# Kernel tuning notes

Measured on AMD Instinct MI355X. Metric: run time of the kernel, lower is better.

## Reference

```python
import math
import jax, jax.numpy as jnp
import numpy as np

FNUM = 64      # exp_channels (fnum)
NHEADS = 4     # num_heads
WS = 8         # window size (both spatial dims)
SHIFT = 4      # cyclic shift (hard-coded in module)
SCALE = FNUM ** -0.5   # NOTE: module scales by fnum**-0.5, not head_dim**-0.5
LN_EPS = 1e-5


def sine_pos_encoding(h, w, num_pos_feats, temperature=10000.0):
    # DETR-style normalized sine position encoding -> (1, h*w, 2*num_pos_feats)
    scale = 2.0 * math.pi
    y = np.cumsum(np.ones((1, h, w), dtype=np.float64), axis=1)
    x = np.cumsum(np.ones((1, h, w), dtype=np.float64), axis=2)
    eps = 1e-6
    y = y / (y[:, -1:, :] + eps) * scale
    x = x / (x[:, :, -1:] + eps) * scale
    dim_t = np.arange(num_pos_feats, dtype=np.float64)
    dim_t = temperature ** (2.0 * (dim_t // 2) / num_pos_feats)
    pos_x = x[..., None] / dim_t
    pos_y = y[..., None] / dim_t
    pos_x = np.stack([np.sin(pos_x[..., 0::2]), np.cos(pos_x[..., 1::2])], axis=-1).reshape(1, h, w, -1)
    pos_y = np.stack([np.sin(pos_y[..., 0::2]), np.cos(pos_y[..., 1::2])], axis=-1).reshape(1, h, w, -1)
    pos = np.concatenate([pos_y, pos_x], axis=-1)
    return jnp.asarray(pos.reshape(1, h * w, 2 * num_pos_feats), dtype=jnp.float32)


def compute_mask_np(H, W, ws, ss):
    # Swin shifted-window attention mask -> (nW, ws*ws, ws*ws) with 0 / -100
    img = np.zeros((H, W))
    cnt = 0
    for hs in (slice(0, -ws), slice(-ws, -ss), slice(-ss, None)):
        for wsl in (slice(0, -ws), slice(-ws, -ss), slice(-ss, None)):
            img[hs, wsl] = cnt
            cnt += 1
    mw = img.reshape(H // ws, ws, W // ws, ws).transpose(0, 2, 1, 3).reshape(-1, ws * ws)
    diff = mw[:, None, :] - mw[:, :, None]
    return jnp.asarray(np.where(diff != 0, -100.0, 0.0), dtype=jnp.float32)


def layernorm(x, w, b):
    m = x.mean(-1, keepdims=True)
    v = x.var(-1, keepdims=True)
    return (x - m) * jax.lax.rsqrt(v + LN_EPS) * w + b


def window_attention(q, k, v, mask):
    # q,k,v: (Bw, nH, N, Ch); mask: (nW, N, N)
    att = jnp.einsum('bhnc,bhmc->bhnm', q * SCALE, k)
    nW, N = mask.shape[0], mask.shape[1]
    att = att.reshape(-1, nW, NHEADS, N, N) + mask[None, :, None]
    att = jax.nn.softmax(att.reshape(-1, NHEADS, N, N), axis=-1)
    out = jnp.einsum('bhnm,bhmc->bnhc', att, v)   # merge heads as (nH C)
    return out.reshape(out.shape[0], N, -1)


def merge_heads(q):
    # (Bw, nH, N, Ch) -> (Bw, N, nH*Ch)
    return q.transpose(0, 2, 1, 3).reshape(q.shape[0], q.shape[2], -1)


def geglu(h, w11, b11, w12, b12, w2, b2):
    return (jax.nn.gelu(h @ w11 + b11, approximate=False) * (h @ w12 + b12)) @ w2 + b2


def reference(x, ln1_w, ln1_b, ln2_w, ln2_b, w_qkv, me_w11, me_b11, me_w12, me_b12, me_w2, me_b2, conv11_w, ff_in_w, ff_dw_w, ff_out_w):
    B, _, C, H, W = x.shape
    nHw, nWw = H // WS, W // WS
    nW = nHw * nWw
    N = WS * WS
    Ch = FNUM // NHEADS
    pos = sine_pos_encoding(WS, WS, FNUM // 2)
    mask = compute_mask_np(H, W, WS, SHIFT)
    x0 = x
    xs = jnp.roll(x, (-SHIFT, -SHIFT), axis=(3, 4))
    # window partition: (B,3,C,H,W) -> (B*3*nW, N, C)
    xw = xs.reshape(B, 3, C, nHw, WS, nWw, WS).transpose(0, 1, 3, 5, 4, 6, 2).reshape(-1, N, C)
    xw = layernorm(xw, ln1_w, ln1_b)
    qkv = (xw + pos) @ w_qkv                                   # (B*3*nW, N, 3F)
    # '(B E nW) W (nP C) -> E nP (B nW) W C'
    qkv = qkv.reshape(B, 3, nW, N, 3, FNUM).transpose(1, 4, 0, 2, 3, 5).reshape(3, 3, B * nW, N, FNUM)
    # '(C nH)' head split: head index is the fast axis (faithful to source)
    qkv = qkv.reshape(3, 3, B * nW, N, Ch, NHEADS).transpose(0, 1, 2, 5, 3, 4)  # (E, P, Bw, nH, N, Ch)
    a1 = window_attention(qkv[1, 0], qkv[0, 1], qkv[0, 2], mask)
    a3 = window_attention(qkv[1, 0], qkv[2, 1], qkv[2, 2], mask)
    a21 = window_attention(qkv[0, 0], qkv[1, 1], qkv[1, 2], mask)
    a21b = window_attention(qkv[0, 0], qkv[2, 1], qkv[2, 2], mask)
    a23 = window_attention(qkv[2, 0], qkv[1, 1], qkv[1, 2], mask)
    a23b = window_attention(qkv[2, 0], qkv[0, 1], qkv[0, 2], mask)
    # keep_query=True path: concat attended features with own query, GEGLU per exposure
    h1 = geglu(jnp.concatenate([a21, a21b, merge_heads(qkv[0, 0])], -1), me_w11[0], me_b11[0], me_w12[0], me_b12[0], me_w2[0], me_b2[0])
    h2 = geglu(jnp.concatenate([a1, a3, merge_heads(qkv[1, 0])], -1), me_w11[1], me_b11[1], me_w12[1], me_b12[1], me_w2[1], me_b2[1])
    h3 = geglu(jnp.concatenate([a23, a23b, merge_heads(qkv[2, 0])], -1), me_w11[2], me_b11[2], me_w12[2], me_b12[2], me_w2[2], me_b2[2])
    xc = jnp.concatenate([h1, h2, h3], 0)                      # (3*B*nW, N, F)
    # window reverse + ffn_dconv 1x1 conv across 3F channels
    xr = xc.reshape(3, B, nHw, nWw, WS, WS, FNUM).transpose(1, 0, 6, 2, 4, 3, 5).reshape(B, 3 * FNUM, H, W)
    xr = jnp.einsum('oi,bihw->bohw', conv11_w, xr).reshape(B, 3, FNUM, H, W)
    xr = jnp.roll(xr, (SHIFT, SHIFT), axis=(3, 4))
    xres = xr + x0
    # FFN: LN over (N C), then GEGLU dwconv FeedForward
    xl = layernorm(xres.transpose(0, 3, 4, 1, 2).reshape(B, H, W, 3 * FNUM), ln2_w, ln2_b)
    xcn = xl.transpose(0, 3, 1, 2)                             # (B, 3F, H, W)
    h = jnp.einsum('oi,bihw->bohw', ff_in_w, xcn)              # (B, 12F, H, W)
    h = jax.lax.conv_general_dilated(h, ff_dw_w[:, None], (1, 1), ((1, 1), (1, 1)),
                                     feature_group_count=h.shape[1],
                                     dimension_numbers=('NCHW', 'OIHW', 'NCHW'))
    g1, g2 = jnp.split(h, 2, axis=1)
    h = jax.nn.gelu(g1, approximate=False) * g2                # (B, 6F, H, W)
    out = jnp.einsum('oi,bihw->bohw', ff_out_w, h).reshape(B, 3, FNUM, H, W)
    return xres + out


def setup_inputs():
    key = jax.random.key(0)
    ks = jax.random.split(key, 10)
    F3, F6, F12 = 3 * FNUM, 6 * FNUM, 12 * FNUM
    def w(k, shape, fan_in):
        return jax.random.normal(k, shape, jnp.float32) * (fan_in ** -0.5)
    return {
        'x': jax.random.normal(ks[0], (1, 3, FNUM, 256, 256), jnp.float32),
        'ln1_w': jnp.ones((FNUM,), jnp.float32),
        'ln1_b': jnp.zeros((FNUM,), jnp.float32),
        'ln2_w': jnp.ones((F3,), jnp.float32),
        'ln2_b': jnp.zeros((F3,), jnp.float32),
        'w_qkv': w(ks[1], (FNUM, F3), FNUM),
        'me_w11': w(ks[2], (3, F3, FNUM), F3),
        'me_b11': jnp.zeros((3, FNUM), jnp.float32),
        'me_w12': w(ks[3], (3, F3, FNUM), F3),
        'me_b12': jnp.zeros((3, FNUM), jnp.float32),
        'me_w2': w(ks[4], (3, FNUM, FNUM), FNUM),
        'me_b2': jnp.zeros((3, FNUM), jnp.float32),
        'conv11_w': w(ks[5], (F3, F3), F3),
        'ff_in_w': w(ks[6], (F12, F3), F3),
        'ff_dw_w': w(ks[7], (F12, 3, 3), 9),
        'ff_out_w': w(ks[8], (F3, F6), F6),
    }
```

## Files before the change

kernel.cpp:

```cpp
#include <hip/hip_runtime.h>
#include <hip/hip_bf16.h>
#include <math.h>

typedef __hip_bfloat16 bf16;
typedef __attribute__((ext_vector_type(8))) short short8;
typedef __attribute__((ext_vector_type(4))) short short4v;
typedef __attribute__((ext_vector_type(4))) float f32x4;

__device__ __forceinline__ float b2f(bf16 v) { return __bfloat162float(v); }
__device__ __forceinline__ bf16 f2b(float v) { return __float2bfloat16(v); }
__device__ __forceinline__ short f2s(float v) { bf16 b = __float2bfloat16(v); return *(short*)&b; }
__device__ __forceinline__ float s2f(short s) { bf16 b = *(bf16*)&s; return __bfloat162float(b); }
__device__ __forceinline__ float gelu_fast(float x) {
  float z = 0.7978845608028654f * x * (1.0f + 0.044715f * x * x);
  float e = __expf(2.0f * z);
  float t = 1.0f - 2.0f / (e + 1.0f);
  return 0.5f * x * (1.0f + t);
}
__device__ __forceinline__ bool detect_f32(const void* ln1w) {
  return *(const unsigned int*)ln1w == 0x3F800000u;
}
__device__ __forceinline__ float ldx(const void* p, int i, bool f32) {
  return f32 ? ((const float*)p)[i] : b2f(((const bf16*)p)[i]);
}
#define MFMA16(a, b, c) __builtin_amdgcn_mfma_f32_16x16x32_bf16((a), (b), (c), 0, 0, 0)

#define OFF_LN1W  0
#define OFF_LN1B  64
#define OFF_LN2W  128
#define OFF_LN2B  320
#define OFF_WQKVT 512
#define OFF_W11T  12800
#define OFF_B11   49664
#define OFF_W12T  49856
#define OFF_B12   86720
#define OFF_W2T   86912
#define OFF_B2    99200
#define OFF_CW    99392
#define OFF_FIW   136256
#define OFF_DWW   283712
#define OFF_FOW   290624

#define QOFF 0
#define KOFF 4352
#define VOFF 9472

__global__ void __launch_bounds__(256) k_convert(
    const void* __restrict__ src, bf16* __restrict__ dst, int n,
    const void* __restrict__ raw) {
  const bool f32 = detect_f32(raw);
  int i = blockIdx.x * 256 + threadIdx.x;
  if (i < n) dst[i] = f2b(ldx(src, i, f32));
}

__global__ void __launch_bounds__(256) k_convT(
    const void* __restrict__ src, bf16* __restrict__ dst, int R, int C, int n,
    const void* __restrict__ raw) {
  const bool f32 = detect_f32(raw);
  int i = blockIdx.x * 256 + threadIdx.x;
  if (i >= n) return;
  int rc = R * C;
  int s = i / rc, rem = i - s * rc;
  int r = rem / C, c = rem - r * C;
  dst[s * rc + c * R + r] = f2b(ldx(src, i, f32));
}

__global__ void __launch_bounds__(256) k_pos(float* __restrict__ posT) {
  int i = blockIdx.x * 256 + threadIdx.x;
  if (i >= 4096) return;
  int t = i >> 6, ch = i & 63;
  int r = t >> 3, c = t & 7;
  int c2 = ch & 31;
  float coord = (ch < 32) ? (float)(r + 1) : (float)(c + 1);
  float base = coord * (6.283185307179586f / 8.000001f);
  int k = c2 >> 1;
  float d = powf(10000.0f, (float)k * (1.0f / 16.0f));
  float a = base / d;
  posT[i] = (c2 & 1) ? cosf(a) : sinf(a);
}

__global__ void __launch_bounds__(256) k_qkv(
    const void* __restrict__ x, const void* __restrict__ raw,
    const bf16* __restrict__ W, const float* __restrict__ posT,
    short* __restrict__ qkvS, int wy0, int NWL) {
  const int e  = blockIdx.x / NWL;
  const int wl = blockIdx.x - e * NWL;
  const int wy = wy0 + (wl >> 5), wx = wl & 31;
  const int tid = threadIdx.x;
  const bool xf32 = detect_f32(raw);

  __shared__ alignas(16) short xln[64 * 72];
  __shared__ alignas(16) short qout[13824];
  __shared__ float mu[64], rs[64];

  for (int i = tid; i < 1024; i += 256) {
    int xq = i & 1, ty = (i >> 1) & 7, ch = i >> 4;
    int y  = (wy * 8 + ty + 4) & 255;
    int xs = (wx * 8 + 4 + xq * 4) & 255;
    size_t gi = ((size_t)(e * 64 + ch) * 256 + y) * 256 + xs;
    float f0, f1, f2, f3;
    if (xf32) {
      f32x4 v4 = *(const f32x4*)((const float*)x + gi);
      f0 = v4[0]; f1 = v4[1]; f2 = v4[2]; f3 = v4[3];
    } else {
      short4v v4 = *(const short4v*)((const bf16*)x + gi);
      f0 = s2f(v4[0]); f1 = s2f(v4[1]); f2 = s2f(v4[2]); f3 = s2f(v4[3]);
    }
    int tb = (ty * 8 + xq * 4) * 72 + ch;
    xln[tb]       = f2s(f0);
    xln[tb + 72]  = f2s(f1);
    xln[tb + 144] = f2s(f2);
    xln[tb + 216] = f2s(f3);
  }
  __syncthreads();
  if (tid < 64) {
    const short* row = xln + tid * 72;
    float s = 0.f, s2 = 0.f;
    #pragma unroll
    for (int k8 = 0; k8 < 8; k8++) {
      short8 v = *(const short8*)(row + k8 * 8);
      #pragma unroll
      for (int j = 0; j < 8; j++) { float f = s2f(v[j]); s += f; s2 += f * f; }
    }
    float m = s * (1.0f / 64.0f);
    float var = s2 * (1.0f / 64.0f) - m * m;
    mu[tid] = m; rs[tid] = rsqrtf(var + 1e-5f);
  }
  __syncthreads();
  for (int u = tid; u < 512; u += 256) {
    int co = u & 7, t = u >> 3;
    int idx = t * 72 + co * 8;
    short8 xv = *(const short8*)(xln + idx);
    float m = mu[t], rr = rs[t];
    const float* pt = posT + t * 64 + co * 8;
    f32x4 pa = *(const f32x4*)pt;
    f32x4 pb = *(const f32x4*)(pt + 4);
    short8 lw = *(const short8*)(const void*)(W + OFF_LN1W + co * 8);
    short8 lb = *(const short8*)(const void*)(W + OFF_LN1B + co * 8);
    short8 o;
    #pragma unroll
    for (int j = 0; j < 8; j++) {
      float p = (j < 4) ? pa[j] : pb[j - 4];
      o[j] = f2s((s2f(xv[j]) - m) * rr * s2f(lw[j]) + s2f(lb[j]) + p);
    }
    *(short8*)(xln + idx) = o;
  }
  __syncthreads();

  const int lid = tid & 63;
  const int w = tid >> 6;
  const int mrow = lid & 15, q = lid >> 4;
  const int t0 = w * 16 + q * 4;
  const int h = mrow & 3;
  const bf16* wqT = W + OFF_WQKVT;
  short8 a0 = *(const short8*)(xln + (w * 16 + mrow) * 72 + q * 8);
  short8 a1 = *(const short8*)(xln + (w * 16 + mrow) * 72 + 32 + q * 8);
  for (int nt = 0; nt < 12; nt++) {
    f32x4 acc = {0.f, 0.f, 0.f, 0.f};
    short8 b0 = *(const short8*)(const void*)(wqT + (nt * 16 + mrow) * 64 + q * 8);
    short8 b1 = *(const short8*)(const void*)(wqT + (nt * 16 + mrow) * 64 + 32 + q * 8);
    acc = MFMA16(a0, b0, acc);
    acc = MFMA16(a1, b1, acc);
    int p = nt >> 2;
    int c = (nt & 3) * 4 + (mrow >> 2);
    if (p == 0) {
      int o2 = h * 16 + c;
      #pragma unroll
      for (int r = 0; r < 4; r++)
        qout[QOFF + (t0 + r) * 68 + o2] = f2s(acc[r]);
    } else if (p == 1) {
      int rb = KOFF + (h * 64 + t0) * 20 + c;
      #pragma unroll
      for (int r = 0; r < 4; r++)
        qout[rb + r * 20] = f2s(acc[r] * 0.125f);
    } else {
      int rb = VOFF + (h * 16 + c) * 68 + q * 16 + w;
      #pragma unroll
      for (int r = 0; r < 4; r++)
        qout[rb + r * 4] = f2s(acc[r]);
    }
  }
  __syncthreads();
  const size_t gb = ((size_t)wl * 9 + e * 3) * 4096;
  for (int u = tid; u < 3072; u += 256) {
    int j = u * 4, p = j >> 12, rem = j & 4095, src;
    if (p == 0)      src = QOFF + (rem >> 6) * 68 + (rem & 63);
    else if (p == 1) src = KOFF + (rem >> 4) * 20 + (rem & 15);
    else             src = VOFF + (rem >> 6) * 68 + (rem & 63);
    *(short4v*)(qkvS + gb + j) = *(const short4v*)(qout + src);
  }
}

__global__ void __launch_bounds__(256, 3) k_attn(
    const short* __restrict__ qkvS, const bf16* __restrict__ W,
    short* __restrict__ xcS, int wy0, int NWL) {
  const int e  = blockIdx.x / NWL;
  const int wl = blockIdx.x - e * NWL;
  const int wy = wy0 + (wl >> 5), wx = wl & 31;
  const int tid = threadIdx.x;

  __shared__ alignas(16) short cat[64 * 200];
  __shared__ alignas(16) short Kh[4096];
  __shared__ alignas(16) short Vt[64 * 72];
  __shared__ alignas(16) short Pb[64 * 72];
  __shared__ alignas(16) short kz[16];
  short* gbuf = Pb;

  const int ea = (e == 0) ? 1 : ((e == 1) ? 0 : 1);
  const int eb = (e == 0) ? 2 : ((e == 1) ? 2 : 0);
  const short* Qg = qkvS + ((size_t)wl * 9 + e * 3 + 0) * 4096;
  const short* Kg[2] = { qkvS + ((size_t)wl * 9 + ea * 3 + 1) * 4096,
                         qkvS + ((size_t)wl * 9 + eb * 3 + 1) * 4096 };
  const short* Vg[2] = { qkvS + ((size_t)wl * 9 + ea * 3 + 2) * 4096,
                         qkvS + ((size_t)wl * 9 + eb * 3 + 2) * 4096 };

  if (tid < 16) kz[tid] = 0;
  for (int i = tid; i < 512; i += 256) {
    int t = i >> 3, ch = i & 7;
    *(short8*)(cat + t * 200 + 128 + ch * 8) = *(const short8*)(Qg + t * 64 + ch * 8);
  }

  const int lid = tid & 63;
  const int w = tid >> 6;
  const int mrow = lid & 15, q = lid >> 4;
  const int masky = (wy == 31), maskx = (wx == 31);
  const bool anymask = (masky | maskx) != 0;
  const short8 zero8 = {0, 0, 0, 0, 0, 0, 0, 0};

  float madd[4][4];
  if (anymask) {
    int qi = w * 16 + mrow;
    int lyi = masky ? (((qi >> 3) < 4) ? 1 : 2) : 0;
    int lxi = maskx ? (((qi & 7) < 4) ? 1 : 2) : 0;
    #pragma unroll
    for (int nt = 0; nt < 4; nt++)
      #pragma unroll
      for (int r = 0; r < 4; r++) {
        int kj = nt * 16 + q * 4 + r;
        int lyj = masky ? (((kj >> 3) < 4) ? 1 : 2) : 0;
        int lxj = maskx ? (((kj & 7) < 4) ? 1 : 2) : 0;
        madd[nt][r] = (lyi != lyj || lxi != lxj) ? -100.0f : 0.0f;
      }
  }

  for (int src = 0; src < 2; src++) {
    if (src) __syncthreads();
    for (int i = tid; i < 512; i += 256)
      *(short8*)(Kh + i * 8) = *(const short8*)(Kg[src] + i * 8);
    for (int i = tid; i < 512; i += 256) {
      int row = i >> 3, ch = i & 7;
      *(short8*)(Vt + row * 72 + ch * 8) = *(const short8*)(Vg[src] + row * 64 + ch * 8);
    }
    __syncthreads();

    for (int h = 0; h < 4; h++) {
      short8 qf = (q < 2)
          ? *(const short8*)(cat + (w * 16 + mrow) * 200 + 128 + h * 16 + q * 8)
          : zero8;
      const short* kb; int kstep;
      if (q < 2) { kb = Kh + (h * 64 + mrow) * 16 + q * 8; kstep = 256; }
      else       { kb = kz; kstep = 0; }
      f32x4 s[4];
      #pragma unroll
      for (int nt = 0; nt < 4; nt++) {
        short8 kf = *(const short8*)(kb + nt * kstep);
        f32x4 z = {0.f, 0.f, 0.f, 0.f};
        s[nt] = MFMA16(kf, qf, z);
      }
      if (anymask) {
        #pragma unroll
        for (int nt = 0; nt < 4; nt++)
          #pragma unroll
          for (int r = 0; r < 4; r++) s[nt][r] += madd[nt][r];
      }
      float mx = s[0][0];
      #pragma unroll
      for (int nt = 0; nt < 4; nt++)
        #pragma unroll
        for (int r = 0; r < 4; r++) if (nt | r) mx = fmaxf(mx, s[nt][r]);
      mx = fmaxf(mx, __shfl_xor(mx, 16));
      mx = fmaxf(mx, __shfl_xor(mx, 32));
      float pr[4][4]; float sum = 0.f;
      #pragma unroll
      for (int nt = 0; nt < 4; nt++)
        #pragma unroll
        for (int r = 0; r < 4; r++) {
          float ev = __expf(s[nt][r] - mx);
          pr[nt][r] = ev; sum += ev;
        }
      sum += __shfl_xor(sum, 16);
      sum += __shfl_xor(sum, 32);
      float inv = 1.0f / sum;
      int ro = (w * 16 + mrow) * 72 + q * 16;
      #pragma unroll
      for (int r = 0; r < 4; r++) {
        short4v pv = { f2s(pr[0][r] * inv), f2s(pr[1][r] * inv),
                       f2s(pr[2][r] * inv), f2s(pr[3][r] * inv) };
        *(short4v*)(Pb + ro + r * 4) = pv;
      }
      asm volatile("s_waitcnt lgkmcnt(0)" ::: "memory");
      f32x4 o = {0.f, 0.f, 0.f, 0.f};
      #pragma unroll
      for (int kc = 0; kc < 2; kc++) {
        short8 pa = *(const short8*)(Pb + (w * 16 + mrow) * 72 + kc * 32 + q * 8);
        short8 vb = *(const short8*)(Vt + (h * 16 + mrow) * 72 + kc * 32 + q * 8);
        o = MFMA16(pa, vb, o);
      }
      #pragma unroll
      for (int r = 0; r < 4; r++)
        cat[(w * 16 + q * 4 + r) * 200 + src * 64 + h * 16 + mrow] = f2s(o[r]);
    }
  }
  __syncthreads();

  {
    short8 a[6];
    #pragma unroll
    for (int kc = 0; kc < 6; kc++)
      a[kc] = *(const short8*)(cat + (w * 16 + mrow) * 200 + kc * 32 + q * 8);
    f32x4 ua[4], va[4];
    const bf16* w1T = W + OFF_W11T + (size_t)e * 64 * 192;
    const bf16* w2T = W + OFF_W12T + (size_t)e * 64 * 192;
    for (int nt = 0; nt < 4; nt++) {
      f32x4 au = {0.f, 0.f, 0.f, 0.f}, av = {0.f, 0.f, 0.f, 0.f};
      #pragma unroll
      for (int kc = 0; kc < 6; kc++) {
        short8 bu = *(const short8*)(const void*)(w1T + (nt * 16 + mrow) * 192 + kc * 32 + q * 8);
        short8 bv = *(const short8*)(const void*)(w2T + (nt * 16 + mrow) * 192 + kc * 32 + q * 8);
        au = MFMA16(a[kc], bu, au);
        av = MFMA16(a[kc], bv, av);
      }
      ua[nt] = au; va[nt] = av;
    }
    for (int nt = 0; nt < 4; nt++) {
      int o = nt * 16 + mrow;
      float bu = b2f(W[OFF_B11 + e * 64 + o]);
      float bv = b2f(W[OFF_B12 + e * 64 + o]);
      #pragma unroll
      for (int r = 0; r < 4; r++)
        gbuf[(w * 16 + q * 4 + r) * 72 + o] = f2s(gelu_fast(ua[nt][r] + bu) * (va[nt][r] + bv));
    }
  }
  {
    short8 g0 = *(const short8*)(gbuf + (w * 16 + mrow) * 72 + q * 8);
    short8 g1 = *(const short8*)(gbuf + (w * 16 + mrow) * 72 + 32 + q * 8);
    const bf16* w2T = W + OFF_W2T + (size_t)e * 64 * 64;
    for (int nt = 0; nt < 4; nt++) {
      f32x4 acc = {0.f, 0.f, 0.f, 0.f};
      short8 b0 = *(const short8*)(const void*)(w2T + (nt * 16 + mrow) * 64 + q * 8);
      short8 b1 = *(const short8*)(const void*)(w2T + (nt * 16 + mrow) * 64 + 32 + q * 8);
      acc = MFMA16(g0, b0, acc);
      acc = MFMA16(g1, b1, acc);
      int o = nt * 16 + mrow;
      float bb = b2f(W[OFF_B2 + e * 64 + o]);
      #pragma unroll
      for (int r = 0; r < 4; r++)
        cat[(w * 16 + q * 4 + r) * 200 + o] = f2s(acc[r] + bb);
    }
  }
  __syncthreads();
  short* xcbase = xcS + ((size_t)wl * 3 + e) * 4096;
  for (int i = tid; i < 1024; i += 256) {
    int tt = i >> 4, f4 = (i & 15) * 4;
    *(short4v*)(xcbase + tt * 64 + f4) = *(const short4v*)(cat + tt * 200 + f4);
  }
}

__global__ void __launch_bounds__(256) k_conv11(
    const short* __restrict__ xcS, const bf16* __restrict__ W,
    const void* __restrict__ x, const void* __restrict__ raw,
    short* __restrict__ xres, int wy0, int NWL) {
  const int wl = blockIdx.x;
  const int wy = wy0 + (wl >> 5), wx = wl & 31;
  const int tid = threadIdx.x;
  const bool xf32 = detect_f32(raw);
  __shared__ alignas(16) short ct[64 * 200];
  __shared__ alignas(16) short xt[64 * 200];

  for (int i = tid; i < 3072; i += 256) {
    int e = i >> 10, rem = i & 1023;
    int tt = rem >> 4, f4 = (rem & 15) * 4;
    *(short4v*)(ct + tt * 200 + e * 64 + f4)
        = *(const short4v*)(xcS + ((size_t)wl * 3 + e) * 4096 + tt * 64 + f4);
  }
  for (int i = tid; i < 3072; i += 256) {
    int xq = i & 1, ty = (i >> 1) & 7, ch = (i >> 4) & 63, e = i >> 10;
    int y  = (wy * 8 + ty + 4) & 255;
    int xs = (wx * 8 + 4 + xq * 4) & 255;
    size_t gi = ((size_t)(e * 64 + ch) * 256 + y) * 256 + xs;
    float f0, f1, f2, f3;
    if (xf32) {
      f32x4 v4 = *(const f32x4*)((const float*)x + gi);
      f0 = v4[0]; f1 = v4[1]; f2 = v4[2]; f3 = v4[3];
    } else {
      short4v v4 = *(const short4v*)((const bf16*)x + gi);
      f0 = s2f(v4[0]); f1 = s2f(v4[1]); f2 = s2f(v4[2]); f3 = s2f(v4[3]);
    }
    int tb = (ty * 8 + xq * 4) * 200 + e * 64 + ch;
    xt[tb]       = f2s(f0);
    xt[tb + 200] = f2s(f1);
    xt[tb + 400] = f2s(f2);
    xt[tb + 600] = f2s(f3);
  }
  __syncthreads();

  const int lid = tid & 63;
  const int w = tid >> 6;
  const int mrow = lid & 15, q = lid >> 4;
  short8 a[6];
  #pragma unroll
  for (int kc = 0; kc < 6; kc++)
    a[kc] = *(const short8*)(ct + (w * 16 + mrow) * 200 + kc * 32 + q * 8);

  const int t = w * 16 + mrow;
  const int ty2 = (wy * 8 + (t >> 3) + 4) & 255;
  const int tx2 = (wx * 8 + (t & 7) + 4) & 255;
  short* xrow = xres + (size_t)(ty2 * 256 + tx2) * 192;
  const short* resrow = xt + t * 200;

  const bf16* cw = W + OFF_CW;
  for (int nt = 0; nt < 12; nt++) {
    f32x4 acc = {0.f, 0.f, 0.f, 0.f};
    #pragma unroll
    for (int kc = 0; kc < 6; kc++) {
      short8 b = *(const short8*)(const void*)(cw + (nt * 16 + mrow) * 192 + kc * 32 + q * 8);
      acc = MFMA16(b, a[kc], acc);
    }
    int o = nt * 16 + q * 4;
    short4v rv = *(const short4v*)(resrow + o);
    short4v o4 = { f2s(acc[0] + s2f(rv[0])), f2s(acc[1] + s2f(rv[1])),
                   f2s(acc[2] + s2f(rv[2])), f2s(acc[3] + s2f(rv[3])) };
    *(short4v*)(xrow + o) = o4;
  }
}

__global__ void __launch_bounds__(256) k_ffin(
    const short* __restrict__ xres, const bf16* __restrict__ W,
    short* __restrict__ hS, int y_start, int y0m1) {
  const int half = blockIdx.x & 1;
  const int idx = blockIdx.x >> 1;
  const int y = y_start + (idx >> 2);
  const int x0 = (idx & 3) * 64;
  const int l = y - y0m1;
  const int tid = threadIdx.x;
  __shared__ alignas(16) short xt[64 * 200];
  __shared__ float mu[64], rs[64];

  for (int i4 = tid; i4 < 3072; i4 += 256) {
    int p = i4 / 48, c4 = (i4 - p * 48) * 4;
    *(short4v*)(xt + p * 200 + c4)
        = *(const short4v*)(xres + (size_t)(y * 256 + x0 + p) * 192 + c4);
  }
  __syncthreads();
  {
    int p = tid >> 2, qd = tid & 3;
    const short* row = xt + p * 200 + qd * 48;
    float s = 0.f, s2 = 0.f;
    #pragma unroll
    for (int k = 0; k < 6; k++) {
      short8 v = *(const short8*)(row + k * 8);
      #pragma unroll
      for (int j = 0; j < 8; j++) { float f = s2f(v[j]); s += f; s2 += f * f; }
    }
    s  += __shfl_xor(s, 1);  s  += __shfl_xor(s, 2);
    s2 += __shfl_xor(s2, 1); s2 += __shfl_xor(s2, 2);
    if (qd == 0) {
      float m = s * (1.0f / 192.0f);
      float var = s2 * (1.0f / 192.0f) - m * m;
      mu[p] = m; rs[p] = rsqrtf(var + 1e-5f);
    }
  }
  __syncthreads();
  for (int u = tid; u < 1536; u += 256) {
    int p = u / 24, c8 = u - p * 24;
    int idx2 = p * 200 + c8 * 8;
    short8 xv = *(const short8*)(xt + idx2);
    float m = mu[p], rr = rs[p];
    short8 lw = *(const short8*)(const void*)(W + OFF_LN2W + c8 * 8);
    short8 lb = *(const short8*)(const void*)(W + OFF_LN2B + c8 * 8);
    short8 o;
    #pragma unroll
    for (int j = 0; j < 8; j++)
      o[j] = f2s((s2f(xv[j]) - m) * rr * s2f(lw[j]) + s2f(lb[j]));
    *(short8*)(xt + idx2) = o;
  }
  __syncthreads();

  const int lid = tid & 63;
  const int m0 = (tid >> 6) * 16;
  const int mrow = lid & 15, q = lid >> 4;
  short8 a[6];
  #pragma unroll
  for (int kc = 0; kc < 6; kc++)
    a[kc] = *(const short8*)(xt + (m0 + mrow) * 200 + kc * 32 + q * 8);

  const bf16* fiw = W + OFF_FIW;
  short* hrow = hS + (size_t)l * 196608 + (size_t)(x0 + m0 + mrow) * 768;
  const int nt0 = half * 24;
  for (int nt = nt0; nt < nt0 + 24; nt++) {
    f32x4 acc = {0.f, 0.f, 0.f, 0.f};
    #pragma unroll
    for (int kc = 0; kc < 6; kc++) {
      short8 b = *(const short8*)(const void*)(fiw + (nt * 16 + mrow) * 192 + kc * 32 + q * 8);
      acc = MFMA16(b, a[kc], acc);
    }
    short4v o4 = { f2s(acc[0]), f2s(acc[1]), f2s(acc[2]), f2s(acc[3]) };
    *(short4v*)(hrow + nt * 16 + q * 4) = o4;
  }
}

__global__ void __launch_bounds__(256) k_ffout(
    const short* __restrict__ hS, const bf16* __restrict__ W,
    const short* __restrict__ xres, void* __restrict__ out,
    const void* __restrict__ raw, int y0, int y0m1) {
  const int y = y0 + (blockIdx.x >> 2);
  const int x0 = (blockIdx.x & 3) * 64;
  const int tid = threadIdx.x;
  const bool of32 = detect_f32(raw);
  __shared__ alignas(16) short ga[64 * 392];

  const bf16* dwwT = W + OFF_DWW;
  const int l = y - y0m1;
  const short8 z8 = {0, 0, 0, 0, 0, 0, 0, 0};
  for (int it = 0; it < 6; it++) {
    int unit = it * 256 + tid;
    int pq = unit / 48, oo = unit - pq * 48;
    int o = oo * 8;
    int xxb = x0 + pq * 2;
    float u0[8] = {0,0,0,0,0,0,0,0}, v0[8] = {0,0,0,0,0,0,0,0};
    float u1[8] = {0,0,0,0,0,0,0,0}, v1[8] = {0,0,0,0,0,0,0,0};
    #pragma unroll
    for (int dy = -1; dy <= 1; dy++) {
      int yy = y + dy;
      if (yy < 0 || yy >= 256) continue;
      const short* rbase = hS + (size_t)(l + dy) * 196608;
      short8 hu[4], hv[4];
      #pragma unroll
      for (int k = 0; k < 4; k++) {
        int xv = xxb - 1 + k;
        if (xv < 0 || xv >= 256) { hu[k] = z8; hv[k] = z8; }
        else {
          const short* hp = rbase + (size_t)xv * 768 + o;
          hu[k] = *(const short8*)(hp);
          hv[k] = *(const short8*)(hp + 384);
        }
      }
      const bf16* wrow = dwwT + (dy + 1) * 3 * 768 + o;
      short8 w0u = *(const short8*)(const void*)(wrow);
      short8 w0v = *(const short8*)(const void*)(wrow + 384);
      short8 w1u = *(const short8*)(const void*)(wrow + 768);
      short8 w1v = *(const short8*)(const void*)(wrow + 768 + 384);
      short8 w2u = *(const short8*)(const void*)(wrow + 1536);
      short8 w2v = *(const short8*)(const void*)(wrow + 1536 + 384);
      #pragma unroll
      for (int j = 0; j < 8; j++) {
        float a0 = s2f(w0u[j]), a1 = s2f(w1u[j]), a2 = s2f(w2u[j]);
        float b0 = s2f(w0v[j]), b1 = s2f(w1v[j]), b2 = s2f(w2v[j]);
        float h0u = s2f(hu[0][j]), h1u = s2f(hu[1][j]), h2u = s2f(hu[2][j]), h3u = s2f(hu[3][j]);
        float h0v = s2f(hv[0][j]), h1v = s2f(hv[1][j]), h2v = s2f(hv[2][j]), h3v = s2f(hv[3][j]);
        u0[j] += a0 * h0u + a1 * h1u + a2 * h2u;
        u1[j] += a0 * h1u + a1 * h2u + a2 * h3u;
        v0[j] += b0 * h0v + b1 * h1v + b2 * h2v;
        v1[j] += b0 * h1v + b1 * h2v + b2 * h3v;
      }
    }
    short8 g0, g1;
    #pragma unroll
    for (int j = 0; j < 8; j++) {
      g0[j] = f2s(gelu_fast(u0[j]) * v0[j]);
      g1[j] = f2s(gelu_fast(u1[j]) * v1[j]);
    }
    *(short8*)(ga + (pq * 2) * 392 + o)     = g0;
    *(short8*)(ga + (pq * 2 + 1) * 392 + o) = g1;
  }
  __syncthreads();

  const int lid = tid & 63;
  const int m0 = (tid >> 6) * 16;
  const int mrow = lid & 15, q = lid >> 4;
  short8 a[12];
  #pragma unroll
  for (int kc = 0; kc < 12; kc++)
    a[kc] = *(const short8*)(ga + (m0 + mrow) * 392 + kc * 32 + q * 8);
  __syncthreads();

  for (int i4 = tid; i4 < 3072; i4 += 256) {
    int pp = i4 / 48, c4 = (i4 - pp * 48) * 4;
    *(short4v*)(ga + pp * 392 + 200 + c4)
        = *(const short4v*)(xres + (size_t)(y * 256 + x0 + pp) * 192 + c4);
  }

  const bf16* fow = W + OFF_FOW;
  for (int nt = 0; nt < 12; nt++) {
    f32x4 acc = {0.f, 0.f, 0.f, 0.f};
    #pragma unroll
    for (int kc = 0; kc < 12; kc++) {
      short8 b = *(const short8*)(const void*)(fow + (nt * 16 + mrow) * 384 + kc * 32 + q * 8);
      acc = MFMA16(a[kc], b, acc);
    }
    #pragma unroll
    for (int r = 0; r < 4; r++)
      ga[(m0 + q * 4 + r) * 392 + nt * 16 + mrow] = f2s(acc[r]);
  }
  __syncthreads();

  for (int it = 0; it < 48; it++) {
    int flat = it * 256 + tid;
    int pp = flat & 63, ch = flat >> 6;
    int idx = ch * 65536 + y * 256 + x0 + pp;
    float r = s2f(ga[pp * 392 + ch]) + s2f(ga[pp * 392 + 200 + ch]);
    if (of32) ((float*)out)[idx] = r;
    else      ((bf16*)out)[idx] = f2b(r);
  }
}

extern "C" void kernel_launch(void* const* d_in, const int* in_sizes, int n_in,
                              void* d_out, int out_size, void* d_ws, size_t ws_size,
                              hipStream_t stream) {
  const void* x   = d_in[0];
  const void* raw = d_in[1];
  char* ws = (char*)d_ws;
  bf16*  W    = (bf16*)(ws + 1024);
  float* posT = (float*)(ws + 786432);
  short* xres = (short*)(ws + 0x100000);
  const size_t ATT = 28ull * 1024 * 1024;

  size_t avail = (ws_size > ATT) ? ws_size - ATT : 0;
  int swr = 32;
  while (swr > 1 && (size_t)swr * 3145728ull > avail) swr >>= 1;
  int hr = 256;
  while (hr > 4 && (size_t)(hr + 2) * 393216ull > avail) hr >>= 1;

  short* qkvS = (short*)(ws + ATT);
  short* xcS  = (short*)(ws + ATT + (size_t)swr * 2359296ull);
  short* hS   = (short*)(ws + ATT);

  { const int di[10]   = {1, 2, 3, 4, 7, 9, 11, 12, 13, 15};
    const int offp[10] = {OFF_LN1W, OFF_LN1B, OFF_LN2W, OFF_LN2B, OFF_B11,
                          OFF_B12, OFF_B2, OFF_CW, OFF_FIW, OFF_FOW};
    const int cnt[10]  = {64, 64, 192, 192, 192, 192, 192, 36864, 147456, 73728};
    for (int i = 0; i < 10; i++)
      k_convert<<<(cnt[i] + 255) / 256, 256, 0, stream>>>(
          d_in[di[i]], W + offp[i], cnt[i], raw);
  }
  k_convT<<<(12288 + 255) / 256, 256, 0, stream>>>(d_in[5], W + OFF_WQKVT, 64, 192, 12288, raw);
  k_convT<<<(36864 + 255) / 256, 256, 0, stream>>>(d_in[6], W + OFF_W11T, 192, 64, 36864, raw);
  k_convT<<<(36864 + 255) / 256, 256, 0, stream>>>(d_in[8], W + OFF_W12T, 192, 64, 36864, raw);
  k_convT<<<(12288 + 255) / 256, 256, 0, stream>>>(d_in[10], W + OFF_W2T, 64, 64, 12288, raw);
  k_convT<<<(6912 + 255) / 256, 256, 0, stream>>>(d_in[14], W + OFF_DWW, 768, 9, 6912, raw);
  k_pos<<<16, 256, 0, stream>>>(posT);

  for (int wy0 = 0; wy0 < 32; wy0 += swr) {
    int NWL = swr * 32;
    k_qkv<<<3 * NWL, 256, 0, stream>>>(x, raw, W, posT, qkvS, wy0, NWL);
    k_attn<<<3 * NWL, 256, 0, stream>>>(qkvS, W, xcS, wy0, NWL);
    k_conv11<<<NWL, 256, 0, stream>>>(xcS, W, x, raw, xres, wy0, NWL);
  }

  for (int y0 = 0; y0 < 256; y0 += hr) {
    int ys = (y0 == 0) ? 0 : (y0 - 1);
    int ye = (y0 + hr > 255) ? 255 : (y0 + hr);
    int nrows = ye - ys + 1;
    k_ffin<<<nrows * 8, 256, 0, stream>>>(xres, W, hS, ys, y0 - 1);
    k_ffout<<<hr * 4, 256, 0, stream>>>(hS, W, xres, d_out, raw, y0, y0 - 1);
  }
}
```

Before: 693.6 us.

## Fuse FF input projection with depthwise conv and gating into one kernel

Replaces k_ffin (LN2 plus the 768-channel input projection, written to a global buffer) and the depthwise/gating half of k_ffout with a new k_gate kernel. Each k_gate block recomputes LN2 and the projection for a 3-row, 66-pixel halo in shared memory, for one 64-channel slice of the u and v halves. It then runs the 3x3 depthwise conv and GELU gating and writes only the 384-channel gate to global memory. k_ffout now just loads the gate and does the output projection. This removes the large 768-channel intermediate round-trip and the row-chunked launch loop, at the cost of redundant LN and projection work across halo rows and channel slices, plus heavy shared memory use per block.

```diff
diff --git a/kernel.cpp b/kernel.cpp
--- a/kernel.cpp
+++ b/kernel.cpp
@@ -434,118 +434,130 @@
   }
 }
 
-__global__ void __launch_bounds__(256) k_ffin(
+#define HST 132
+__global__ void __launch_bounds__(256) k_gate(
     const short* __restrict__ xres, const bf16* __restrict__ W,
-    short* __restrict__ hS, int y_start, int y0m1) {
-  const int half = blockIdx.x & 1;
-  const int idx = blockIdx.x >> 1;
-  const int y = y_start + (idx >> 2);
-  const int x0 = (idx & 3) * 64;
-  const int l = y - y0m1;
+    short* __restrict__ gateS) {
+  const int b = blockIdx.x;
+  const int y = b / 24;
+  const int rem = b - y * 24;
+  const int xs = rem / 6, cs = rem - xs * 6;
+  const int x0 = xs * 64;
+  const int gc0 = cs * 64;
   const int tid = threadIdx.x;
-  __shared__ alignas(16) short xt[64 * 200];
-  __shared__ float mu[64], rs[64];
-
-  for (int i4 = tid; i4 < 3072; i4 += 256) {
-    int p = i4 / 48, c4 = (i4 - p * 48) * 4;
-    *(short4v*)(xt + p * 200 + c4)
-        = *(const short4v*)(xres + (size_t)(y * 256 + x0 + p) * 192 + c4);
-  }
-  __syncthreads();
+
+  __shared__ alignas(16) short xln[66 * 200];
+  __shared__ alignas(16) short hbuf[3 * 66 * HST];
+  __shared__ float mu[66], rs[66];
+
+  const int lid = tid & 63;
+  const int wv = tid >> 6;
+  const int mrow = lid & 15, q = lid >> 4;
+  const bf16* fiw = W + OFF_FIW;
+  const short8 z8 = {0, 0, 0, 0, 0, 0, 0, 0};
+
+  for (int rr = 0; rr < 3; rr++) {
+    if (rr) __syncthreads();
+    int yy = y - 1 + rr;
+    short* hb = hbuf + rr * 66 * HST;
+    if (yy < 0 || yy > 255) {
+      for (int i = tid; i < 1089; i += 256)
+        if (i * 8 <= 66 * HST - 8) *(short8*)(hb + i * 8) = z8;
+      continue;
+    }
+    for (int u = tid; u < 3168; u += 256) {
+      int p = u / 48, c4 = (u - p * 48) * 4;
+      int xg = x0 - 1 + p;
+      xg = xg < 0 ? 0 : (xg > 255 ? 255 : xg);
+      *(short4v*)(xln + p * 200 + c4)
+          = *(const short4v*)(xres + ((size_t)yy * 256 + xg) * 192 + c4);
+    }
+    __syncthreads();
+    {
+      int p = tid >> 1, qd = tid & 1;
+      if (p < 66) {
+        const short* row = xln + p * 200 + qd * 96;
+        float s = 0.f, s2 = 0.f;
+        #pragma unroll
+        for (int k = 0; k < 12; k++) {
+          short8 v = *(const short8*)(row + k * 8);
+          #pragma unroll
+          for (int j = 0; j < 8; j++) { float f = s2f(v[j]); s += f; s2 += f * f; }
+        }
+        s += __shfl_xor(s, 1); s2 += __shfl_xor(s2, 1);
+        if (qd == 0) {
+          float m = s * (1.0f / 192.0f);
+          float var = s2 * (1.0f / 192.0f) - m * m;
+          mu[p] = m; rs[p] = rsqrtf(var + 1e-5f);
+        }
+      }
+    }
+    __syncthreads();
+    for (int u = tid; u < 1584; u += 256) {
+      int p = u / 24, c8 = u - p * 24;
+      int idx = p * 200 + c8 * 8;
+      short8 xv = *(const short8*)(xln + idx);
+      float m = mu[p], rr2 = rs[p];
+      short8 lw = *(const short8*)(const void*)(W + OFF_LN2W + c8 * 8);
+      short8 lb = *(const short8*)(const void*)(W + OFF_LN2B + c8 * 8);
+      short8 o;
+      #pragma unroll
+      for (int j = 0; j < 8; j++)
+        o[j] = f2s((s2f(xv[j]) - m) * rr2 * s2f(lw[j]) + s2f(lb[j]));
+      *(short8*)(xln + idx) = o;
+    }
+    __syncthreads();
+    for (int tile = wv; tile < 5; tile += 4) {
+      int rt = tile * 16 + mrow;
+      int rc = rt < 66 ? rt : 65;
+      short8 a[6];
+      #pragma unroll
+      for (int kc = 0; kc < 6; kc++)
+        a[kc] = *(const short8*)(xln + rc * 200 + kc * 32 + q * 8);
+      for (int nt = 0; nt < 8; nt++) {
+        int hc = (nt < 4) ? (gc0 + nt * 16 + mrow)
+                          : (gc0 + 384 + (nt - 4) * 16 + mrow);
+        f32x4 acc = {0.f, 0.f, 0.f, 0.f};
+        #pragma unroll
+        for (int kc = 0; kc < 6; kc++) {
+          short8 bw = *(const short8*)(const void*)(fiw + (size_t)hc * 192 + kc * 32 + q * 8);
+          acc = MFMA16(bw, a[kc], acc);
+        }
+        if (rt < 66) {
+          short4v o4 = { f2s(acc[0]), f2s(acc[1]), f2s(acc[2]), f2s(acc[3]) };
+          *(short4v*)(hb + rt * HST + nt * 16 + q * 4) = o4;
+        }
+      }
+    }
+  }
+  __syncthreads();
+  if (x0 == 0 && tid < 48) {
+    int rr = tid >> 4, c8 = tid & 15;
+    *(short8*)(hbuf + rr * 66 * HST + 0 * HST + c8 * 8) = z8;
+  }
+  if (x0 == 192 && tid < 48) {
+    int rr = tid >> 4, c8 = tid & 15;
+    *(short8*)(hbuf + rr * 66 * HST + 65 * HST + c8 * 8) = z8;
+  }
+  __syncthreads();
+
   {
-    int p = tid >> 2, qd = tid & 3;
-    const short* row = xt + p * 200 + qd * 48;
-    float s = 0.f, s2 = 0.f;
-    #pragma unroll
-    for (int k = 0; k < 6; k++) {
-      short8 v = *(const short8*)(row + k * 8);
-      #pragma unroll
-      for (int j = 0; j < 8; j++) { float f = s2f(v[j]); s += f; s2 += f * f; }
-    }
-    s  += __shfl_xor(s, 1);  s  += __shfl_xor(s, 2);
-    s2 += __shfl_xor(s2, 1); s2 += __shfl_xor(s2, 2);
-    if (qd == 0) {
-      float m = s * (1.0f / 192.0f);
-      float var = s2 * (1.0f / 192.0f) - m * m;
-      mu[p] = m; rs[p] = rsqrtf(var + 1e-5f);
-    }
-  }
-  __syncthreads();
-  for (int u = tid; u < 1536; u += 256) {
-    int p = u / 24, c8 = u - p * 24;
-    int idx2 = p * 200 + c8 * 8;
-    short8 xv = *(const short8*)(xt + idx2);
-    float m = mu[p], rr = rs[p];
-    short8 lw = *(const short8*)(const void*)(W + OFF_LN2W + c8 * 8);
-    short8 lb = *(const short8*)(const void*)(W + OFF_LN2B + c8 * 8);
-    short8 o;
-    #pragma unroll
-    for (int j = 0; j < 8; j++)
-      o[j] = f2s((s2f(xv[j]) - m) * rr * s2f(lw[j]) + s2f(lb[j]));
-    *(short8*)(xt + idx2) = o;
-  }
-  __syncthreads();
-
-  const int lid = tid & 63;
-  const int m0 = (tid >> 6) * 16;
-  const int mrow = lid & 15, q = lid >> 4;
-  short8 a[6];
-  #pragma unroll
-  for (int kc = 0; kc < 6; kc++)
-    a[kc] = *(const short8*)(xt + (m0 + mrow) * 200 + kc * 32 + q * 8);
-
-  const bf16* fiw = W + OFF_FIW;
-  short* hrow = hS + (size_t)l * 196608 + (size_t)(x0 + m0 + mrow) * 768;
-  const int nt0 = half * 24;
-  for (int nt = nt0; nt < nt0 + 24; nt++) {
-    f32x4 acc = {0.f, 0.f, 0.f, 0.f};
-    #pragma unroll
-    for (int kc = 0; kc < 6; kc++) {
-      short8 b = *(const short8*)(const void*)(fiw + (nt * 16 + mrow) * 192 + kc * 32 + q * 8);
-      acc = MFMA16(b, a[kc], acc);
-    }
-    short4v o4 = { f2s(acc[0]), f2s(acc[1]), f2s(acc[2]), f2s(acc[3]) };
-    *(short4v*)(hrow + nt * 16 + q * 4) = o4;
-  }
-}
-
-__global__ void __launch_bounds__(256) k_ffout(
-    const short* __restrict__ hS, const bf16* __restrict__ W,
-    const short* __restrict__ xres, void* __restrict__ out,
-    const void* __restrict__ raw, int y0, int y0m1) {
-  const int y = y0 + (blockIdx.x >> 2);
-  const int x0 = (blockIdx.x & 3) * 64;
-  const int tid = threadIdx.x;
-  const bool of32 = detect_f32(raw);
-  __shared__ alignas(16) short ga[64 * 392];
-
-  const bf16* dwwT = W + OFF_DWW;
-  const int l = y - y0m1;
-  const short8 z8 = {0, 0, 0, 0, 0, 0, 0, 0};
-  for (int it = 0; it < 6; it++) {
-    int unit = it * 256 + tid;
-    int pq = unit / 48, oo = unit - pq * 48;
-    int o = oo * 8;
-    int xxb = x0 + pq * 2;
+    const bf16* dwwT = W + OFF_DWW;
+    int pq = tid >> 3, oo = tid & 7;
+    int p0 = pq * 2;
     float u0[8] = {0,0,0,0,0,0,0,0}, v0[8] = {0,0,0,0,0,0,0,0};
     float u1[8] = {0,0,0,0,0,0,0,0}, v1[8] = {0,0,0,0,0,0,0,0};
     #pragma unroll
-    for (int dy = -1; dy <= 1; dy++) {
-      int yy = y + dy;
-      if (yy < 0 || yy >= 256) continue;
-      const short* rbase = hS + (size_t)(l + dy) * 196608;
+    for (int rr = 0; rr < 3; rr++) {
+      const short* hb = hbuf + rr * 66 * HST;
       short8 hu[4], hv[4];
       #pragma unroll
       for (int k = 0; k < 4; k++) {
-        int xv = xxb - 1 + k;
-        if (xv < 0 || xv >= 256) { hu[k] = z8; hv[k] = z8; }
-        else {
-          const short* hp = rbase + (size_t)xv * 768 + o;
-          hu[k] = *(const short8*)(hp);
-          hv[k] = *(const short8*)(hp + 384);
-        }
-      }
-      const bf16* wrow = dwwT + (dy + 1) * 3 * 768 + o;
+        const short* hp = hb + (p0 + k) * HST + oo * 8;
+        hu[k] = *(const short8*)(hp);
+        hv[k] = *(const short8*)(hp + 64);
+      }
+      const bf16* wrow = dwwT + rr * 3 * 768 + gc0 + oo * 8;
       short8 w0u = *(const short8*)(const void*)(wrow);
       short8 w0v = *(const short8*)(const void*)(wrow + 384);
       short8 w1u = *(const short8*)(const void*)(wrow + 768);
@@ -570,8 +582,26 @@
       g0[j] = f2s(gelu_fast(u0[j]) * v0[j]);
       g1[j] = f2s(gelu_fast(u1[j]) * v1[j]);
     }
-    *(short8*)(ga + (pq * 2) * 392 + o)     = g0;
-    *(short8*)(ga + (pq * 2 + 1) * 392 + o) = g1;
+    size_t gb = ((size_t)y * 256 + x0 + p0) * 384 + gc0 + oo * 8;
+    *(short8*)(gateS + gb) = g0;
+    *(short8*)(gateS + gb + 384) = g1;
+  }
+}
+
+__global__ void __launch_bounds__(256) k_ffout(
+    const short* __restrict__ gateS, const bf16* __restrict__ W,
+    const short* __restrict__ xres, void* __restrict__ out,
+    const void* __restrict__ raw) {
+  const int y = blockIdx.x >> 2;
+  const int x0 = (blockIdx.x & 3) * 64;
+  const int tid = threadIdx.x;
+  const bool of32 = detect_f32(raw);
+  __shared__ alignas(16) short ga[64 * 392];
+
+  for (int u = tid; u < 3072; u += 256) {
+    int p = u / 48, c8 = u - p * 48;
+    *(short8*)(ga + p * 392 + c8 * 8)
+        = *(const short8*)(gateS + ((size_t)(y * 256 + x0 + p)) * 384 + c8 * 8);
   }
   __syncthreads();
 
@@ -628,12 +658,10 @@
   size_t avail = (ws_size > ATT) ? ws_size - ATT : 0;
   int swr = 32;
   while (swr > 1 && (size_t)swr * 3145728ull > avail) swr >>= 1;
-  int hr = 256;
-  while (hr > 4 && (size_t)(hr + 2) * 393216ull > avail) hr >>= 1;
-
-  short* qkvS = (short*)(ws + ATT);
-  short* xcS  = (short*)(ws + ATT + (size_t)swr * 2359296ull);
-  short* hS   = (short*)(ws + ATT);
+
+  short* qkvS  = (short*)(ws + ATT);
+  short* xcS   = (short*)(ws + ATT + (size_t)swr * 2359296ull);
+  short* gateS = (short*)(ws + ATT);
 
   { const int di[10]   = {1, 2, 3, 4, 7, 9, 11, 12, 13, 15};
     const int offp[10] = {OFF_LN1W, OFF_LN1B, OFF_LN2W, OFF_LN2B, OFF_B11,
@@ -657,11 +685,6 @@
     k_conv11<<<NWL, 256, 0, stream>>>(xcS, W, x, raw, xres, wy0, NWL);
   }
 
-  for (int y0 = 0; y0 < 256; y0 += hr) {
-    int ys = (y0 == 0) ? 0 : (y0 - 1);
-    int ye = (y0 + hr > 255) ? 255 : (y0 + hr);
-    int nrows = ye - ys + 1;
-    k_ffin<<<nrows * 8, 256, 0, stream>>>(xres, W, hS, ys, y0 - 1);
-    k_ffout<<<hr * 4, 256, 0, stream>>>(hS, W, xres, d_out, raw, y0, y0 - 1);
-  }
-}
+  k_gate<<<256 * 24, 256, 0, stream>>>(xres, W, gateS);
+  k_ffout<<<1024, 256, 0, stream>>>(gateS, W, xres, d_out, raw);
+}
```

Result: slower. 1.371 ms (+97.6%).
